# Kernel optimization log

Measured on AMD Instinct MI355X. Metric: run time of the kernel, lower is better.

## Reference

```python
import jax, jax.numpy as jnp
import numpy as np
import math

D_MODEL = 128
B, H, S, D = 4, 16, 2048, 128

def setup_inputs() -> dict:
    key = jax.random.key(0)
    kq, kk, kv, km = jax.random.split(key, 4)
    q = jax.random.normal(kq, (B, H, S, D), dtype=jnp.float32)
    k = jax.random.normal(kk, (B, H, S, D), dtype=jnp.float32)
    v = jax.random.normal(kv, (B, H, S, D), dtype=jnp.float32)
    mask = jax.random.randint(km, (1, 1, S, S), 0, 2, dtype=jnp.int32)
    return {"q": q, "k": k, "v": v, "mask": mask}

def reference(q, k, v, mask):
    scale = 1.0 / math.sqrt(D_MODEL)
    # [B,H,S,S] score matrix (faithful to the unfused original)
    scores = jnp.einsum('bhsd,bhtd->bhst', q, k) * scale
    neg = jnp.finfo(scores.dtype).min
    scores = jnp.where(mask == 0, neg, scores)
    attn = jax.nn.softmax(scores, axis=-1)
    return jnp.einsum('bhst,bhtd->bhsd', attn, v)
```

## Files before the change

### kernel.cpp

```cpp
#include <hip/hip_runtime.h>
#include <hip/hip_bf16.h>
#include <stdint.h>

#define S_LEN 2048
#define D_HEAD 128
#define TILE_T 64
#define QTILE 128
#define N_TILES (S_LEN / TILE_T)

typedef __attribute__((ext_vector_type(8))) __bf16 bf16x8;
typedef __attribute__((ext_vector_type(4))) float f32x4;
typedef __attribute__((ext_vector_type(4))) float fvec4;

#define KS_STRIDE 136
#define VS_STRIDE 72
#define PS_STRIDE 72

__device__ __forceinline__ __bf16 to_bf16_rne(float f) {
    unsigned u = __builtin_bit_cast(unsigned, f);
    u += 0x7FFFu + ((u >> 16) & 1u);
    unsigned short h = (unsigned short)(u >> 16);
    return __builtin_bit_cast(__bf16, h);
}

__global__ __launch_bounds__(256, 2)
void sdpa_flash_kernel(const float* __restrict__ q,
                       const float* __restrict__ k,
                       const float* __restrict__ v,
                       const int*   __restrict__ mask,
                       float* __restrict__ out)
{
    __shared__ __align__(16) __bf16 Ks[TILE_T * KS_STRIDE];
    __shared__ __align__(16) __bf16 Vtmp[TILE_T * D_HEAD];
    __shared__ __align__(16) __bf16 Vs[D_HEAD * VS_STRIDE];
    __shared__ __align__(16) __bf16 Ps[QTILE * PS_STRIDE];

    const int tid  = threadIdx.x;
    const int wave = tid >> 6;
    const int lane = tid & 63;
    const int quad = lane >> 4;
    const int lc   = lane & 15;

    const int q0 = blockIdx.x * QTILE;
    const int bh = blockIdx.y;

    const float* qbh = q + (size_t)bh * S_LEN * D_HEAD;
    const float* kbh = k + (size_t)bh * S_LEN * D_HEAD;
    const float* vbh = v + (size_t)bh * S_LEN * D_HEAD;

    bf16x8 qf[2][4];
    #pragma unroll
    for (int mt = 0; mt < 2; ++mt) {
        const float* qrow = qbh + (size_t)(q0 + wave * 32 + mt * 16 + lc) * D_HEAD + quad * 8;
        #pragma unroll
        for (int kc = 0; kc < 4; ++kc) {
            fvec4 a = *(const fvec4*)(qrow + kc * 32);
            fvec4 b = *(const fvec4*)(qrow + kc * 32 + 4);
            bf16x8 f;
            #pragma unroll
            for (int j = 0; j < 4; ++j) {
                f[j]     = to_bf16_rne(a[j]);
                f[4 + j] = to_bf16_rne(b[j]);
            }
            qf[mt][kc] = f;
        }
    }

    f32x4 o_acc[2][8];
    #pragma unroll
    for (int mt = 0; mt < 2; ++mt)
        #pragma unroll
        for (int i = 0; i < 8; ++i) o_acc[mt][i] = (f32x4){0.f, 0.f, 0.f, 0.f};
    float l_lane[2][4];
    #pragma unroll
    for (int mt = 0; mt < 2; ++mt)
        #pragma unroll
        for (int r = 0; r < 4; ++r) l_lane[mt][r] = 0.f;

    const float scale = 0.08838834764831845f;

    for (int kt = 0; kt < N_TILES; ++kt) {
        __syncthreads();

        int mk[2][4][4];
        #pragma unroll
        for (int mt = 0; mt < 2; ++mt) {
            const int* mbase = mask + (size_t)(q0 + wave * 32 + mt * 16 + quad * 4) * S_LEN
                                    + (size_t)kt * TILE_T + lc;
            #pragma unroll
            for (int r = 0; r < 4; ++r)
                #pragma unroll
                for (int nt = 0; nt < 4; ++nt)
                    mk[mt][r][nt] = mbase[(size_t)r * S_LEN + nt * 16];
        }

        {
            const float* kg = kbh + (size_t)kt * TILE_T * D_HEAD;
            const float* vg = vbh + (size_t)kt * TILE_T * D_HEAD;
            #pragma unroll
            for (int i = 0; i < 4; ++i) {
                int idx = tid + i * 256;
                int r  = idx >> 4;
                int c8 = (idx & 15) << 3;
                fvec4 ka = *(const fvec4*)(kg + r * D_HEAD + c8);
                fvec4 kb = *(const fvec4*)(kg + r * D_HEAD + c8 + 4);
                fvec4 va = *(const fvec4*)(vg + r * D_HEAD + c8);
                fvec4 vb = *(const fvec4*)(vg + r * D_HEAD + c8 + 4);
                bf16x8 kw, vw;
                #pragma unroll
                for (int j = 0; j < 4; ++j) {
                    kw[j]     = to_bf16_rne(ka[j]);
                    kw[4 + j] = to_bf16_rne(kb[j]);
                    vw[j]     = to_bf16_rne(va[j]);
                    vw[4 + j] = to_bf16_rne(vb[j]);
                }
                *(bf16x8*)(&Ks[r * KS_STRIDE + c8]) = kw;
                *(bf16x8*)(&Vtmp[r * D_HEAD + c8])  = vw;
            }
        }
        __syncthreads();

        {
            int t0 = (tid >> 5) << 3;
            int d0 = (tid & 31) << 2;
            uint2 w[8];
            #pragma unroll
            for (int j = 0; j < 8; ++j)
                w[j] = *(const uint2*)(&Vtmp[(t0 + j) * D_HEAD + d0]);
            #pragma unroll
            for (int e = 0; e < 4; ++e) {
                uint32_t row[4];
                #pragma unroll
                for (int p = 0; p < 4; ++p) {
                    uint32_t a = (e & 2) ? w[2*p].y   : w[2*p].x;
                    uint32_t b = (e & 2) ? w[2*p+1].y : w[2*p+1].x;
                    row[p] = (e & 1) ? ((a >> 16) | (b & 0xFFFF0000u))
                                     : ((a & 0xFFFFu) | (b << 16));
                }
                *(uint4*)(&Vs[(d0 + e) * VS_STRIDE + t0]) = *(uint4*)row;
            }
        }

        f32x4 s_acc[2][4];
        #pragma unroll
        for (int mt = 0; mt < 2; ++mt)
            #pragma unroll
            for (int nt = 0; nt < 4; ++nt) s_acc[mt][nt] = (f32x4){0.f, 0.f, 0.f, 0.f};
        #pragma unroll
        for (int nt = 0; nt < 4; ++nt)
            #pragma unroll
            for (int kc = 0; kc < 4; ++kc) {
                bf16x8 kf = *(const bf16x8*)(&Ks[(nt * 16 + lc) * KS_STRIDE + kc * 32 + quad * 8]);
                s_acc[0][nt] = __builtin_amdgcn_mfma_f32_16x16x32_bf16(qf[0][kc], kf, s_acc[0][nt], 0, 0, 0);
                s_acc[1][nt] = __builtin_amdgcn_mfma_f32_16x16x32_bf16(qf[1][kc], kf, s_acc[1][nt], 0, 0, 0);
            }

        #pragma unroll
        for (int mt = 0; mt < 2; ++mt) {
            __bf16* pw = &Ps[(wave * 32 + mt * 16) * PS_STRIDE];
            #pragma unroll
            for (int nt = 0; nt < 4; ++nt)
                #pragma unroll
                for (int r = 0; r < 4; ++r) {
                    float sv = s_acc[mt][nt][r] * scale;
                    float ev = mk[mt][r][nt] ? __expf(sv) : 0.0f;
                    __bf16 eb = to_bf16_rne(ev);
                    l_lane[mt][r] += (float)eb;
                    pw[(quad * 4 + r) * PS_STRIDE + nt * 16 + lc] = eb;
                }
        }

        __syncthreads();

        #pragma unroll
        for (int c = 0; c < 2; ++c) {
            bf16x8 af0 = *(const bf16x8*)(&Ps[(wave * 32 + lc) * PS_STRIDE + c * 32 + quad * 8]);
            bf16x8 af1 = *(const bf16x8*)(&Ps[(wave * 32 + 16 + lc) * PS_STRIDE + c * 32 + quad * 8]);
            #pragma unroll
            for (int dt = 0; dt < 8; ++dt) {
                bf16x8 vf = *(const bf16x8*)(&Vs[(dt * 16 + lc) * VS_STRIDE + c * 32 + quad * 8]);
                o_acc[0][dt] = __builtin_amdgcn_mfma_f32_16x16x32_bf16(af0, vf, o_acc[0][dt], 0, 0, 0);
                o_acc[1][dt] = __builtin_amdgcn_mfma_f32_16x16x32_bf16(af1, vf, o_acc[1][dt], 0, 0, 0);
            }
        }
    }

    #pragma unroll
    for (int mt = 0; mt < 2; ++mt)
        #pragma unroll
        for (int r = 0; r < 4; ++r) {
            float s = l_lane[mt][r];
            #pragma unroll
            for (int off = 1; off < 16; off <<= 1)
                s += __shfl_xor(s, off, 64);
            l_lane[mt][r] = s;
        }

    float* obh = out + (size_t)bh * S_LEN * D_HEAD;
    #pragma unroll
    for (int mt = 0; mt < 2; ++mt)
        #pragma unroll
        for (int r = 0; r < 4; ++r) {
            float inv = 1.0f / l_lane[mt][r];
            const size_t row = (size_t)(q0 + wave * 32 + mt * 16 + quad * 4 + r) * D_HEAD;
            #pragma unroll
            for (int dt = 0; dt < 8; ++dt)
                obh[row + dt * 16 + lc] = o_acc[mt][dt][r] * inv;
        }
}

extern "C" void kernel_launch(void* const* d_in, const int* in_sizes, int n_in,
                              void* d_out, int out_size, void* d_ws, size_t ws_size,
                              hipStream_t stream)
{
    const float* q    = (const float*)d_in[0];
    const float* k    = (const float*)d_in[1];
    const float* v    = (const float*)d_in[2];
    const int*   mask = (const int*)d_in[3];
    float* out = (float*)d_out;

    dim3 grid(S_LEN / QTILE, 4 * 16);
    sdpa_flash_kernel<<<grid, 256, 0, stream>>>(q, k, v, mask, out);
}
```

Measured before the change: 554.7 us.

## Bit-pack the mask in a prepass, swizzle LDS tiles, and remap the grid

Adds a prepass kernel that packs the int32 mask into 64-bit ballot words in the workspace. The attention kernel then reads one word per row per key tile instead of sixteen int32 loads per lane, which sharply cuts mask traffic. LDS padding is replaced by an XOR swizzle, and the Vtmp staging buffer is dropped by transposing V directly from global memory. One barrier between the P write and the P read is removed, which relies on each wave reading only its own P rows. Less LDS allows three blocks per CU, and a linear grid remap groups blocks of the same heads together for L2 reuse. The cost is an extra kernel launch and a pass over the full mask on every call.

```diff
diff --git a/kernel.cpp b/kernel.cpp
--- a/kernel.cpp
+++ b/kernel.cpp
@@ -7,14 +7,11 @@
 #define TILE_T 64
 #define QTILE 128
 #define N_TILES (S_LEN / TILE_T)
+#define NBH 64
 
 typedef __attribute__((ext_vector_type(8))) __bf16 bf16x8;
 typedef __attribute__((ext_vector_type(4))) float f32x4;
 typedef __attribute__((ext_vector_type(4))) float fvec4;
-
-#define KS_STRIDE 136
-#define VS_STRIDE 72
-#define PS_STRIDE 72
 
 __device__ __forceinline__ __bf16 to_bf16_rne(float f) {
     unsigned u = __builtin_bit_cast(unsigned, f);
@@ -23,17 +20,28 @@
     return __builtin_bit_cast(__bf16, h);
 }
 
-__global__ __launch_bounds__(256, 2)
+__device__ __forceinline__ int swz(int row, int elem) {
+    return elem ^ (((row ^ (row >> 3)) & 7) << 3);
+}
+
+__global__ void pack_mask_kernel(const int* __restrict__ mask,
+                                 unsigned long long* __restrict__ bits)
+{
+    const int i = blockIdx.x * 256 + threadIdx.x;
+    const unsigned long long b = __ballot(mask[i] != 0);
+    if ((threadIdx.x & 63) == 0) bits[i >> 6] = b;
+}
+
+__global__ __launch_bounds__(256, 3)
 void sdpa_flash_kernel(const float* __restrict__ q,
                        const float* __restrict__ k,
                        const float* __restrict__ v,
-                       const int*   __restrict__ mask,
+                       const unsigned long long* __restrict__ mbits,
                        float* __restrict__ out)
 {
-    __shared__ __align__(16) __bf16 Ks[TILE_T * KS_STRIDE];
-    __shared__ __align__(16) __bf16 Vtmp[TILE_T * D_HEAD];
-    __shared__ __align__(16) __bf16 Vs[D_HEAD * VS_STRIDE];
-    __shared__ __align__(16) __bf16 Ps[QTILE * PS_STRIDE];
+    __shared__ __align__(16) __bf16 Ks[TILE_T * D_HEAD];
+    __shared__ __align__(16) __bf16 Vs[D_HEAD * TILE_T];
+    __shared__ __align__(16) __bf16 Ps[QTILE * TILE_T];
 
     const int tid  = threadIdx.x;
     const int wave = tid >> 6;
@@ -41,8 +49,10 @@
     const int quad = lane >> 4;
     const int lc   = lane & 15;
 
-    const int q0 = blockIdx.x * QTILE;
-    const int bh = blockIdx.y;
+    const int lin = blockIdx.x;
+    const int sub = lin >> 3;
+    const int bh  = (lin & 7) + ((sub >> 4) << 3);
+    const int q0  = (sub & 15) * QTILE;
 
     const float* qbh = q + (size_t)bh * S_LEN * D_HEAD;
     const float* kbh = k + (size_t)bh * S_LEN * D_HEAD;
@@ -82,64 +92,55 @@
     for (int kt = 0; kt < N_TILES; ++kt) {
         __syncthreads();
 
-        int mk[2][4][4];
-        #pragma unroll
-        for (int mt = 0; mt < 2; ++mt) {
-            const int* mbase = mask + (size_t)(q0 + wave * 32 + mt * 16 + quad * 4) * S_LEN
-                                    + (size_t)kt * TILE_T + lc;
-            #pragma unroll
-            for (int r = 0; r < 4; ++r)
-                #pragma unroll
-                for (int nt = 0; nt < 4; ++nt)
-                    mk[mt][r][nt] = mbase[(size_t)r * S_LEN + nt * 16];
-        }
-
         {
             const float* kg = kbh + (size_t)kt * TILE_T * D_HEAD;
-            const float* vg = vbh + (size_t)kt * TILE_T * D_HEAD;
             #pragma unroll
             for (int i = 0; i < 4; ++i) {
-                int idx = tid + i * 256;
-                int r  = idx >> 4;
-                int c8 = (idx & 15) << 3;
-                fvec4 ka = *(const fvec4*)(kg + r * D_HEAD + c8);
-                fvec4 kb = *(const fvec4*)(kg + r * D_HEAD + c8 + 4);
-                fvec4 va = *(const fvec4*)(vg + r * D_HEAD + c8);
-                fvec4 vb = *(const fvec4*)(vg + r * D_HEAD + c8 + 4);
-                bf16x8 kw, vw;
+                const int idx = tid + i * 256;
+                const int r   = idx >> 4;
+                const int c8  = (idx & 15) << 3;
+                fvec4 a = *(const fvec4*)(kg + r * D_HEAD + c8);
+                fvec4 b = *(const fvec4*)(kg + r * D_HEAD + c8 + 4);
+                bf16x8 kw;
                 #pragma unroll
                 for (int j = 0; j < 4; ++j) {
-                    kw[j]     = to_bf16_rne(ka[j]);
-                    kw[4 + j] = to_bf16_rne(kb[j]);
-                    vw[j]     = to_bf16_rne(va[j]);
-                    vw[4 + j] = to_bf16_rne(vb[j]);
+                    kw[j]     = to_bf16_rne(a[j]);
+                    kw[4 + j] = to_bf16_rne(b[j]);
                 }
-                *(bf16x8*)(&Ks[r * KS_STRIDE + c8]) = kw;
-                *(bf16x8*)(&Vtmp[r * D_HEAD + c8])  = vw;
-            }
-        }
-        __syncthreads();
+                *(bf16x8*)(&Ks[swz(r, (r << 7) + c8)]) = kw;
+            }
+        }
 
         {
-            int t0 = (tid >> 5) << 3;
-            int d0 = (tid & 31) << 2;
-            uint2 w[8];
+            const float* vg = vbh + (size_t)kt * TILE_T * D_HEAD;
+            const int t0 = (tid >> 5) << 3;
+            const int d0 = (tid & 31) << 2;
+            fvec4 w4[8];
             #pragma unroll
             for (int j = 0; j < 8; ++j)
-                w[j] = *(const uint2*)(&Vtmp[(t0 + j) * D_HEAD + d0]);
+                w4[j] = *(const fvec4*)(vg + (size_t)(t0 + j) * D_HEAD + d0);
             #pragma unroll
             for (int e = 0; e < 4; ++e) {
-                uint32_t row[4];
+                uint32_t rp[4];
                 #pragma unroll
                 for (int p = 0; p < 4; ++p) {
-                    uint32_t a = (e & 2) ? w[2*p].y   : w[2*p].x;
-                    uint32_t b = (e & 2) ? w[2*p+1].y : w[2*p+1].x;
-                    row[p] = (e & 1) ? ((a >> 16) | (b & 0xFFFF0000u))
-                                     : ((a & 0xFFFFu) | (b << 16));
+                    const unsigned ha = (unsigned)__builtin_bit_cast(unsigned short, to_bf16_rne(w4[2 * p][e]));
+                    const unsigned hb = (unsigned)__builtin_bit_cast(unsigned short, to_bf16_rne(w4[2 * p + 1][e]));
+                    rp[p] = ha | (hb << 16);
                 }
-                *(uint4*)(&Vs[(d0 + e) * VS_STRIDE + t0]) = *(uint4*)row;
-            }
-        }
+                const int d = d0 + e;
+                *(uint4*)(&Vs[swz(d, (d << 6) + t0)]) = *(const uint4*)rp;
+            }
+        }
+
+        __syncthreads();
+
+        unsigned long long mk64[2][4];
+        #pragma unroll
+        for (int mt = 0; mt < 2; ++mt)
+            #pragma unroll
+            for (int r = 0; r < 4; ++r)
+                mk64[mt][r] = mbits[(size_t)(q0 + wave * 32 + mt * 16 + quad * 4 + r) * N_TILES + kt];
 
         f32x4 s_acc[2][4];
         #pragma unroll
@@ -150,35 +151,42 @@
         for (int nt = 0; nt < 4; ++nt)
             #pragma unroll
             for (int kc = 0; kc < 4; ++kc) {
-                bf16x8 kf = *(const bf16x8*)(&Ks[(nt * 16 + lc) * KS_STRIDE + kc * 32 + quad * 8]);
+                const int rk = nt * 16 + lc;
+                bf16x8 kf = *(const bf16x8*)(&Ks[swz(rk, (rk << 7) + kc * 32 + quad * 8)]);
                 s_acc[0][nt] = __builtin_amdgcn_mfma_f32_16x16x32_bf16(qf[0][kc], kf, s_acc[0][nt], 0, 0, 0);
                 s_acc[1][nt] = __builtin_amdgcn_mfma_f32_16x16x32_bf16(qf[1][kc], kf, s_acc[1][nt], 0, 0, 0);
             }
 
         #pragma unroll
-        for (int mt = 0; mt < 2; ++mt) {
-            __bf16* pw = &Ps[(wave * 32 + mt * 16) * PS_STRIDE];
-            #pragma unroll
-            for (int nt = 0; nt < 4; ++nt)
+        for (int mt = 0; mt < 2; ++mt)
+            #pragma unroll
+            for (int r = 0; r < 4; ++r) {
+                const uint32_t lo = (uint32_t)(mk64[mt][r]);
+                const uint32_t hi = (uint32_t)(mk64[mt][r] >> 32);
+                const int prow = wave * 32 + mt * 16 + quad * 4 + r;
                 #pragma unroll
-                for (int r = 0; r < 4; ++r) {
-                    float sv = s_acc[mt][nt][r] * scale;
-                    float ev = mk[mt][r][nt] ? __expf(sv) : 0.0f;
-                    __bf16 eb = to_bf16_rne(ev);
+                for (int nt = 0; nt < 4; ++nt) {
+                    const uint32_t h   = (nt & 2) ? hi : lo;
+                    const uint32_t bit = (h >> ((nt & 1) * 16 + lc)) & 1u;
+                    const float sv = s_acc[mt][nt][r] * scale;
+                    const float ev = bit ? __expf(sv) : 0.0f;
+                    const __bf16 eb = to_bf16_rne(ev);
                     l_lane[mt][r] += (float)eb;
-                    pw[(quad * 4 + r) * PS_STRIDE + nt * 16 + lc] = eb;
+                    Ps[swz(prow, (prow << 6) + nt * 16 + lc)] = eb;
                 }
-        }
-
-        __syncthreads();
+            }
+
 
         #pragma unroll
         for (int c = 0; c < 2; ++c) {
-            bf16x8 af0 = *(const bf16x8*)(&Ps[(wave * 32 + lc) * PS_STRIDE + c * 32 + quad * 8]);
-            bf16x8 af1 = *(const bf16x8*)(&Ps[(wave * 32 + 16 + lc) * PS_STRIDE + c * 32 + quad * 8]);
+            const int ra0 = wave * 32 + lc;
+            const int ra1 = wave * 32 + 16 + lc;
+            bf16x8 af0 = *(const bf16x8*)(&Ps[swz(ra0, (ra0 << 6) + c * 32 + quad * 8)]);
+            bf16x8 af1 = *(const bf16x8*)(&Ps[swz(ra1, (ra1 << 6) + c * 32 + quad * 8)]);
             #pragma unroll
             for (int dt = 0; dt < 8; ++dt) {
-                bf16x8 vf = *(const bf16x8*)(&Vs[(dt * 16 + lc) * VS_STRIDE + c * 32 + quad * 8]);
+                const int rv = dt * 16 + lc;
+                bf16x8 vf = *(const bf16x8*)(&Vs[swz(rv, (rv << 6) + c * 32 + quad * 8)]);
                 o_acc[0][dt] = __builtin_amdgcn_mfma_f32_16x16x32_bf16(af0, vf, o_acc[0][dt], 0, 0, 0);
                 o_acc[1][dt] = __builtin_amdgcn_mfma_f32_16x16x32_bf16(af1, vf, o_acc[1][dt], 0, 0, 0);
             }
@@ -219,6 +227,8 @@
     const int*   mask = (const int*)d_in[3];
     float* out = (float*)d_out;
 
-    dim3 grid(S_LEN / QTILE, 4 * 16);
-    sdpa_flash_kernel<<<grid, 256, 0, stream>>>(q, k, v, mask, out);
-}
+    unsigned long long* mbits = (unsigned long long*)d_ws;
+
+    pack_mask_kernel<<<dim3(S_LEN * S_LEN / 256), 256, 0, stream>>>(mask, mbits);
+    sdpa_flash_kernel<<<dim3((S_LEN / QTILE) * NBH), 256, 0, stream>>>(q, k, v, mbits, out);
+}
```

New measurement: 1.222 ms. +120.3%, slower.
